# Kernel tuning notes

Hardware: AMD Instinct MI355X
Metric: run time of the kernel (lower is better)

## Reference

```python
import jax, jax.numpy as jnp
import numpy as np

NEG_SLOPE = 0.2    # DenseGATConv attention leaky_relu slope (PyG default)
ACT_SLOPE = 0.01   # block activation LeakyReLU slope
HEADS = 3


def setup_inputs() -> dict:
    key = jax.random.key(0)
    B, N, D0, D1, D2, H = 512, 128, 128, 64, 64, HEADS
    ks = jax.random.split(key, 7)
    x = jax.random.normal(ks[0], (B * N, D0), jnp.float32)
    # equal-sized graphs: sorted graph ids, N atoms per graph
    batch_mask = jnp.repeat(jnp.arange(B, dtype=jnp.int32), N)
    s0 = 1.0 / np.sqrt(D0)
    s1 = 1.0 / np.sqrt(D1)
    s2 = 1.0 / np.sqrt(D2)
    W1 = jax.random.normal(ks[1], (D0, H * D1), jnp.float32) * s0
    att_src1 = jax.random.normal(ks[2], (H, D1), jnp.float32) * s1
    att_dst1 = jax.random.normal(ks[3], (H, D1), jnp.float32) * s1
    b1 = jnp.zeros((D1,), jnp.float32)
    W2 = jax.random.normal(ks[4], (D1, H * D2), jnp.float32) * s1
    att_src2 = jax.random.normal(ks[5], (H, D2), jnp.float32) * s2
    att_dst2 = jax.random.normal(ks[6], (H, D2), jnp.float32) * s2
    b2 = jnp.zeros((D2,), jnp.float32)
    return dict(x=x, batch_mask=batch_mask, W1=W1, att_src1=att_src1,
                att_dst1=att_dst1, b1=b1, W2=W2, att_src2=att_src2,
                att_dst2=att_dst2, b2=b2, batch_size=B, n_max=N)


def _dense_gat(x, adj, W, a_src, a_dst, b):
    # x: [B, N, Din], adj: [B, N, N] (self-loops already set). concat=False.
    B, N, _ = x.shape
    H, C = a_src.shape
    h = (x @ W).reshape(B, N, H, C)                       # lin (no bias)
    a_s = jnp.einsum('bnhc,hc->bnh', h, a_src)            # per-node src score
    a_d = jnp.einsum('bnhc,hc->bnh', h, a_dst)            # per-node dst score
    alpha = a_s[:, None, :, :] + a_d[:, :, None, :]       # [B, i, j, H]
    alpha = jax.nn.leaky_relu(alpha, NEG_SLOPE)
    alpha = jnp.where(adj[..., None] == 0, -jnp.inf, alpha)
    alpha = jax.nn.softmax(alpha, axis=2)                 # over source j
    out = jnp.einsum('bijh,bjhc->bihc', alpha, h)         # [B, N, H, C]
    return out.mean(axis=2) + b                           # concat=False -> head mean


def reference(x, batch_mask, W1, att_src1, att_dst1, b1,
              W2, att_src2, att_dst2, b2, batch_size, n_max):
    total, D0 = x.shape
    counts = jnp.bincount(batch_mask, length=batch_size)          # atoms per graph
    starts = jnp.cumsum(counts) - counts
    pos = jnp.arange(total) - starts[batch_mask]                  # slot within graph
    # to_dense_batch
    xd = jnp.zeros((batch_size, n_max, D0), x.dtype).at[batch_mask, pos].set(x)
    node_in = jnp.arange(n_max)[None, :] < counts[:, None]        # [B, N] valid mask
    # block adjacency: fully connected within each graph, diag zeroed...
    adj = (node_in[:, :, None] & node_in[:, None, :]).astype(x.dtype)
    # ...then DenseGATConv add_loop=True re-sets the full diagonal to 1
    adj = jnp.where(jnp.eye(n_max, dtype=bool), jnp.asarray(1.0, x.dtype), adj)
    h = _dense_gat(xd, adj, W1, att_src1, att_dst1, b1)
    h = jax.nn.leaky_relu(h, ACT_SLOPE)
    h = _dense_gat(h, adj, W2, att_src2, att_dst2, b2)
    h = jax.nn.leaky_relu(h, ACT_SLOPE)
    return jnp.sum(h, axis=1)                                     # sum pooling -> [B, D2]
```

## Files before the change

kernel.cpp:

```cpp
#include <hip/hip_runtime.h>
#include <stdint.h>

#define NROW 128
#define HCC  192

typedef __attribute__((ext_vector_type(8))) __bf16 bf16x8;
typedef __attribute__((ext_vector_type(4))) float  f32x4;

static __device__ __forceinline__ uint16_t f2bf(float f) {
    union { float f; uint32_t i; } v; v.f = f;
    uint32_t x = v.i;
    return (uint16_t)((x + 0x7FFFu + ((x >> 16) & 1u)) >> 16);
}
static __device__ __forceinline__ uint16_t bfbits(float f) {
    __bf16 h = (__bf16)f;
    union { __bf16 h; uint16_t u; } c; c.h = h; return c.u;
}

__global__ __launch_bounds__(256)
void prep_kernel(const float* __restrict__ W1, const float* __restrict__ W2,
                 uint16_t* __restrict__ wT1, uint16_t* __restrict__ wT2)
{
    int bid = blockIdx.x, t = threadIdx.x;
    if (bid < 96) {
        int idx = bid * 256 + t;
        int c = idx >> 7, k = idx & 127;
        wT1[c * 128 + k] = f2bf(W1[k * HCC + c]);
    } else {
        int idx = (bid - 96) * 256 + t;
        int c = idx >> 6, k = idx & 63;
        wT2[c * 64 + k] = f2bf(W2[k * HCC + c]);
    }
}

#define HS 136
#define S2 72

static __device__ __forceinline__
void scores_and_hT(const f32x4* hacc, const float* attS, const float* attD,
                   uint16_t* hT, float* as_s, float* ad_s,
                   int i0, int lr, int lg)
{
    float ps[12], pd[12];
#pragma unroll
    for (int q = 0; q < 12; ++q) { ps[q] = 0.f; pd[q] = 0.f; }
#pragma unroll
    for (int f = 0; f < 12; ++f) {
        int hd = f >> 2;
        float av = attS[f * 16 + lr], dv = attD[f * 16 + lr];
#pragma unroll
        for (int r = 0; r < 4; ++r) {
            float hv = hacc[f][r];
            ps[hd * 4 + r] += hv * av;
            pd[hd * 4 + r] += hv * dv;
        }
    }
#pragma unroll
    for (int off = 1; off < 16; off <<= 1)
#pragma unroll
        for (int q = 0; q < 12; ++q) {
            ps[q] += __shfl_xor(ps[q], off);
            pd[q] += __shfl_xor(pd[q], off);
        }
    if (lr == 0) {
#pragma unroll
        for (int hd = 0; hd < 3; ++hd)
#pragma unroll
            for (int r = 0; r < 4; ++r) {
                as_s[hd * 128 + i0 + lg * 4 + r] = ps[hd * 4 + r];
                ad_s[hd * 128 + i0 + lg * 4 + r] = pd[hd * 4 + r];
            }
    }
#pragma unroll
    for (int f = 0; f < 12; ++f) {
        uint32_t p0 = (uint32_t)bfbits(hacc[f][0]) | ((uint32_t)bfbits(hacc[f][1]) << 16);
        uint32_t p1 = (uint32_t)bfbits(hacc[f][2]) | ((uint32_t)bfbits(hacc[f][3]) << 16);
        *(uint2*)&hT[(f * 16 + lr) * HS + i0 + lg * 4] = make_uint2(p0, p1);
    }
}

static __device__ __forceinline__
void softmax_pv(const uint16_t* hT, const float* as_s, const float* ad_s,
                f32x4* oacc, int i0, int l, int lr, int lg)
{
#pragma unroll
    for (int f = 0; f < 4; ++f) oacc[f] = (f32x4){0.f, 0.f, 0.f, 0.f};

    float mxh[3];
#pragma unroll
    for (int hd = 0; hd < 3; ++hd) {
        float a0 = as_s[hd * 128 + l], a1 = as_s[hd * 128 + l + 64];
        mxh[hd] = fmaxf(a0, a1);
    }
#pragma unroll
    for (int off = 1; off < 64; off <<= 1)
#pragma unroll
        for (int hd = 0; hd < 3; ++hd) mxh[hd] = fmaxf(mxh[hd], __shfl_xor(mxh[hd], off));

    for (int hd = 0; hd < 3; ++hd) {
        float ad = ad_s[hd * 128 + i0 + lr];
        float m0 = mxh[hd] + ad;
        float mi = fmaxf(m0, 0.2f * m0);

        float e[4][8];
        float zp = 0.f;
#pragma unroll
        for (int q = 0; q < 4; ++q) {
            float4 s0 = *(const float4*)&as_s[hd * 128 + q * 32 + lg * 8];
            float4 s1 = *(const float4*)&as_s[hd * 128 + q * 32 + lg * 8 + 4];
            float sv[8] = {s0.x, s0.y, s0.z, s0.w, s1.x, s1.y, s1.z, s1.w};
#pragma unroll
            for (int m = 0; m < 8; ++m) {
                float tt = sv[m] + ad;
                tt = fmaxf(tt, 0.2f * tt);
                float ev = __expf(tt - mi);
                e[q][m] = ev; zp += ev;
            }
        }
        zp += __shfl_xor(zp, 16);
        zp += __shfl_xor(zp, 32);
        float inv = 1.0f / zp;
        bf16x8 ap[4];
#pragma unroll
        for (int q = 0; q < 4; ++q)
#pragma unroll
            for (int m = 0; m < 8; ++m) ap[q][m] = (__bf16)(e[q][m] * inv);
#pragma unroll
        for (int q = 0; q < 4; ++q)
#pragma unroll
            for (int f = 0; f < 4; ++f) {
                bf16x8 bfv = *(const bf16x8*)&hT[(hd * 64 + f * 16 + lr) * HS + q * 32 + lg * 8];
                oacc[f] = __builtin_amdgcn_mfma_f32_16x16x32_bf16(ap[q], bfv, oacc[f], 0, 0, 0);
            }
    }
}

__global__ __launch_bounds__(512, 4)
void fused_kernel(const float* __restrict__ x,
                  const uint16_t* __restrict__ wT1g, const uint16_t* __restrict__ wT2g,
                  const float* __restrict__ as1g, const float* __restrict__ ad1g,
                  const float* __restrict__ b1g,
                  const float* __restrict__ as2g, const float* __restrict__ ad2g,
                  const float* __restrict__ b2g,
                  float* __restrict__ outp)
{
    __shared__ __align__(16) uint16_t buf[HCC * HS];
    __shared__ __align__(16) float as_s[3 * 128];
    __shared__ __align__(16) float ad_s[3 * 128];
    __shared__ float attS[2][HCC], attD[2][HCC], bia[2][64];
    __shared__ float pool_s[8 * 64];

    uint16_t* wT1l = buf;
    uint16_t* hT   = buf;
    uint16_t* x2T  = buf;
    uint16_t* wT2l = buf + 128 * S2;

    const int b = blockIdx.x, t = threadIdx.x;
    const int w = t >> 6, l = t & 63, lr = l & 15, lg = l >> 4;
    const int i0 = w * 16;

    bf16x8 afr[4];
    {
        const float* xg = x + ((long)b * NROW + i0 + lr) * 128;
        float4 r0[4], r1[4];
#pragma unroll
        for (int q = 0; q < 4; ++q) {
            r0[q] = *(const float4*)(xg + q * 32 + lg * 8);
            r1[q] = *(const float4*)(xg + q * 32 + lg * 8 + 4);
        }
#pragma unroll
        for (int q = 0; q < 4; ++q) {
            bf16x8 a;
            a[0] = (__bf16)r0[q].x; a[1] = (__bf16)r0[q].y;
            a[2] = (__bf16)r0[q].z; a[3] = (__bf16)r0[q].w;
            a[4] = (__bf16)r1[q].x; a[5] = (__bf16)r1[q].y;
            a[6] = (__bf16)r1[q].z; a[7] = (__bf16)r1[q].w;
            afr[q] = a;
        }
    }
#pragma unroll
    for (int p = 0; p < 6; ++p) {
        int idx = t + p * 512; int row = idx >> 4; int c8 = (idx & 15) * 8;
        *(uint4*)&wT1l[row * HS + c8] = *(const uint4*)(wT1g + row * 128 + c8);
    }
    if (t < 192)      { attS[0][t] = as1g[t]; attD[0][t] = ad1g[t]; }
    else if (t < 384) { attS[1][t - 192] = as2g[t - 192]; attD[1][t - 192] = ad2g[t - 192]; }
    else if (t < 448) bia[0][t - 384] = b1g[t - 384];
    else              bia[1][t - 448] = b2g[t - 448];
    __syncthreads();

    f32x4 hacc[12];
#pragma unroll
    for (int f = 0; f < 12; ++f) hacc[f] = (f32x4){0.f, 0.f, 0.f, 0.f};
#pragma unroll
    for (int q = 0; q < 4; ++q) {
#pragma unroll
        for (int f = 0; f < 12; ++f) {
            bf16x8 bfv = *(const bf16x8*)&wT1l[(f * 16 + lr) * HS + q * 32 + lg * 8];
            hacc[f] = __builtin_amdgcn_mfma_f32_16x16x32_bf16(afr[q], bfv, hacc[f], 0, 0, 0);
        }
    }
    __syncthreads();

    scores_and_hT(hacc, attS[0], attD[0], hT, as_s, ad_s, i0, lr, lg);
    __syncthreads();

    uint4 wpre[3];
#pragma unroll
    for (int p = 0; p < 3; ++p) {
        int idx = t + p * 512; int row = idx >> 3; int c8 = (idx & 7) * 8;
        wpre[p] = *(const uint4*)(wT2g + row * 64 + c8);
    }

    f32x4 oacc[4];
    softmax_pv(hT, as_s, ad_s, oacc, i0, l, lr, lg);
    __syncthreads();

    {
        const float inv3 = 1.f / 3.f;
#pragma unroll
        for (int f = 0; f < 4; ++f) {
            int c = f * 16 + lr;
            float bv = bia[0][c];
#pragma unroll
            for (int r = 0; r < 4; ++r) {
                float v = oacc[f][r] * inv3 + bv;
                v = fmaxf(v, 0.01f * v);
                x2T[(i0 + lg * 4 + r) * S2 + c] = bfbits(v);
            }
        }
#pragma unroll
        for (int p = 0; p < 3; ++p) {
            int idx = t + p * 512; int row = idx >> 3; int c8 = (idx & 7) * 8;
            *(uint4*)&wT2l[row * S2 + c8] = wpre[p];
        }
    }
    __syncthreads();

#pragma unroll
    for (int f = 0; f < 12; ++f) hacc[f] = (f32x4){0.f, 0.f, 0.f, 0.f};
#pragma unroll
    for (int q = 0; q < 2; ++q) {
        bf16x8 af = *(const bf16x8*)&x2T[(i0 + lr) * S2 + q * 32 + lg * 8];
#pragma unroll
        for (int f = 0; f < 12; ++f) {
            bf16x8 bfv = *(const bf16x8*)&wT2l[(f * 16 + lr) * S2 + q * 32 + lg * 8];
            hacc[f] = __builtin_amdgcn_mfma_f32_16x16x32_bf16(af, bfv, hacc[f], 0, 0, 0);
        }
    }
    __syncthreads();

    scores_and_hT(hacc, attS[1], attD[1], hT, as_s, ad_s, i0, lr, lg);
    __syncthreads();

    softmax_pv(hT, as_s, ad_s, oacc, i0, l, lr, lg);

    {
        const float inv3 = 1.f / 3.f;
#pragma unroll
        for (int f = 0; f < 4; ++f) {
            int c = f * 16 + lr;
            float bv = bia[1][c];
            float s = 0.f;
#pragma unroll
            for (int r = 0; r < 4; ++r) {
                float v = oacc[f][r] * inv3 + bv;
                v = fmaxf(v, 0.01f * v);
                s += v;
            }
            s += __shfl_xor(s, 16);
            s += __shfl_xor(s, 32);
            if (lg == 0) pool_s[w * 64 + c] = s;
        }
    }
    __syncthreads();
    if (t < 64) {
        float s = 0.f;
#pragma unroll
        for (int q = 0; q < 8; ++q) s += pool_s[q * 64 + t];
        outp[(long)b * 64 + t] = s;
    }
}

extern "C" void kernel_launch(void* const* d_in, const int* in_sizes, int n_in,
                              void* d_out, int out_size, void* d_ws, size_t ws_size,
                              hipStream_t stream)
{
    const float* x   = (const float*)d_in[0];
    const float* W1  = (const float*)d_in[2];
    const float* as1 = (const float*)d_in[3];
    const float* ad1 = (const float*)d_in[4];
    const float* b1  = (const float*)d_in[5];
    const float* W2  = (const float*)d_in[6];
    const float* as2 = (const float*)d_in[7];
    const float* ad2 = (const float*)d_in[8];
    const float* b2  = (const float*)d_in[9];

    uint16_t* wT1 = (uint16_t*)d_ws;
    uint16_t* wT2 = wT1 + 192 * 128;

    prep_kernel<<<144, 256, 0, stream>>>(W1, W2, wT1, wT2);
    fused_kernel<<<512, 512, 0, stream>>>(x, wT1, wT2, as1, ad1, b1, as2, ad2, b2,
                                          (float*)d_out);
}
```

Baseline: 131.7 us.

## Fold attention vectors into weights and defer softmax normalization

Precomputes W·att_src and W·att_dst per head in the prep kernel (scaled by log2e) and appends them as 16 extra output columns, so the attention scores come out of the projection MFMA instead of a shuffle-reduction pass. Softmax now uses exp2 and applies the 1/(3·Z) normalization after the PV MFMA through a per-row reciprocal shuffle, which also absorbs the head-mean scaling. This removes the score reductions and the per-element normalization multiplies, at the cost of one extra MFMA column tile per projection. Scores are now rounded to bf16, which reduces their precision.

```diff
diff --git a/kernel.cpp b/kernel.cpp
--- a/kernel.cpp
+++ b/kernel.cpp
@@ -2,7 +2,6 @@
 #include <stdint.h>
 
 #define NROW 128
-#define HCC  192
 
 typedef __attribute__((ext_vector_type(8))) __bf16 bf16x8;
 typedef __attribute__((ext_vector_type(4))) float  f32x4;
@@ -16,20 +15,74 @@
     __bf16 h = (__bf16)f;
     union { __bf16 h; uint16_t u; } c; c.h = h; return c.u;
 }
+static __device__ __forceinline__ float fexp2(float x) {
+#if __has_builtin(__builtin_amdgcn_exp2f)
+    return __builtin_amdgcn_exp2f(x);
+#else
+    return exp2f(x);
+#endif
+}
+static __device__ __forceinline__ float frcp(float x) {
+#if __has_builtin(__builtin_amdgcn_rcpf)
+    return __builtin_amdgcn_rcpf(x);
+#else
+    return 1.0f / x;
+#endif
+}
 
 __global__ __launch_bounds__(256)
-void prep_kernel(const float* __restrict__ W1, const float* __restrict__ W2,
-                 uint16_t* __restrict__ wT1, uint16_t* __restrict__ wT2)
-{
+void prep_kernel(const float* __restrict__ W1, const float* __restrict__ as1,
+                 const float* __restrict__ ad1,
+                 const float* __restrict__ W2, const float* __restrict__ as2,
+                 const float* __restrict__ ad2,
+                 uint16_t* __restrict__ wT1x, uint16_t* __restrict__ wT2x)
+{
+    constexpr float LOG2E = 1.4426950408889634f;
     int bid = blockIdx.x, t = threadIdx.x;
     if (bid < 96) {
         int idx = bid * 256 + t;
         int c = idx >> 7, k = idx & 127;
-        wT1[c * 128 + k] = f2bf(W1[k * HCC + c]);
-    } else {
+        wT1x[c * 128 + k] = f2bf(W1[k * 192 + c]);
+    } else if (bid < 144) {
         int idx = (bid - 96) * 256 + t;
         int c = idx >> 6, k = idx & 63;
-        wT2[c * 64 + k] = f2bf(W2[k * HCC + c]);
+        wT2x[c * 64 + k] = f2bf(W2[k * 192 + c]);
+    } else if (bid == 144) {
+#pragma unroll
+        for (int e = 0; e < 3; ++e) {
+            int idx = t + e * 256;
+            if (idx < 768) {
+                int j = idx >> 7, k = idx & 127, hd = j >> 1;
+                const float* av = (j & 1) ? ad1 : as1;
+                float s = 0.f;
+                for (int c = 0; c < 64; ++c)
+                    s += W1[k * 192 + hd * 64 + c] * av[hd * 64 + c];
+                wT1x[(192 + j) * 128 + k] = f2bf(s * LOG2E);
+            }
+        }
+#pragma unroll
+        for (int e = 0; e < 5; ++e) {
+            int idx = t + e * 256;
+            if (idx < 1280) wT1x[198 * 128 + idx] = 0;
+        }
+    } else {
+#pragma unroll
+        for (int e = 0; e < 2; ++e) {
+            int idx = t + e * 256;
+            if (idx < 384) {
+                int j = idx >> 6, k = idx & 63, hd = j >> 1;
+                const float* av = (j & 1) ? ad2 : as2;
+                float s = 0.f;
+                for (int c = 0; c < 64; ++c)
+                    s += W2[k * 192 + hd * 64 + c] * av[hd * 64 + c];
+                wT2x[(192 + j) * 64 + k] = f2bf(s * LOG2E);
+            }
+        }
+#pragma unroll
+        for (int e = 0; e < 3; ++e) {
+            int idx = t + e * 256;
+            if (idx < 640) wT2x[198 * 64 + idx] = 0;
+        }
     }
 }
 
@@ -37,39 +90,15 @@
 #define S2 72
 
 static __device__ __forceinline__
-void scores_and_hT(const f32x4* hacc, const float* attS, const float* attD,
-                   uint16_t* hT, float* as_s, float* ad_s,
+void scores_and_hT(const f32x4* hacc, uint16_t* hT, float* as_s, float* ad_s,
                    int i0, int lr, int lg)
 {
-    float ps[12], pd[12];
-#pragma unroll
-    for (int q = 0; q < 12; ++q) { ps[q] = 0.f; pd[q] = 0.f; }
-#pragma unroll
-    for (int f = 0; f < 12; ++f) {
-        int hd = f >> 2;
-        float av = attS[f * 16 + lr], dv = attD[f * 16 + lr];
-#pragma unroll
-        for (int r = 0; r < 4; ++r) {
-            float hv = hacc[f][r];
-            ps[hd * 4 + r] += hv * av;
-            pd[hd * 4 + r] += hv * dv;
-        }
-    }
-#pragma unroll
-    for (int off = 1; off < 16; off <<= 1)
-#pragma unroll
-        for (int q = 0; q < 12; ++q) {
-            ps[q] += __shfl_xor(ps[q], off);
-            pd[q] += __shfl_xor(pd[q], off);
-        }
-    if (lr == 0) {
-#pragma unroll
-        for (int hd = 0; hd < 3; ++hd)
-#pragma unroll
-            for (int r = 0; r < 4; ++r) {
-                as_s[hd * 128 + i0 + lg * 4 + r] = ps[hd * 4 + r];
-                ad_s[hd * 128 + i0 + lg * 4 + r] = pd[hd * 4 + r];
-            }
+    if (lr < 6) {
+        float* dst = (lr & 1) ? ad_s : as_s;
+        int hd = lr >> 1;
+#pragma unroll
+        for (int r = 0; r < 4; ++r)
+            dst[hd * 128 + i0 + lg * 4 + r] = hacc[12][r];
     }
 #pragma unroll
     for (int f = 0; f < 12; ++f) {
@@ -88,10 +117,8 @@
 
     float mxh[3];
 #pragma unroll
-    for (int hd = 0; hd < 3; ++hd) {
-        float a0 = as_s[hd * 128 + l], a1 = as_s[hd * 128 + l + 64];
-        mxh[hd] = fmaxf(a0, a1);
-    }
+    for (int hd = 0; hd < 3; ++hd)
+        mxh[hd] = fmaxf(as_s[hd * 128 + l], as_s[hd * 128 + l + 64]);
 #pragma unroll
     for (int off = 1; off < 64; off <<= 1)
 #pragma unroll
@@ -101,8 +128,7 @@
         float ad = ad_s[hd * 128 + i0 + lr];
         float m0 = mxh[hd] + ad;
         float mi = fmaxf(m0, 0.2f * m0);
-
-        float e[4][8];
+        bf16x8 ap[4];
         float zp = 0.f;
 #pragma unroll
         for (int q = 0; q < 4; ++q) {
@@ -113,41 +139,45 @@
             for (int m = 0; m < 8; ++m) {
                 float tt = sv[m] + ad;
                 tt = fmaxf(tt, 0.2f * tt);
-                float ev = __expf(tt - mi);
-                e[q][m] = ev; zp += ev;
+                float ev = fexp2(tt - mi);
+                zp += ev;
+                ap[q][m] = (__bf16)ev;
             }
         }
         zp += __shfl_xor(zp, 16);
         zp += __shfl_xor(zp, 32);
-        float inv = 1.0f / zp;
-        bf16x8 ap[4];
-#pragma unroll
-        for (int q = 0; q < 4; ++q)
-#pragma unroll
-            for (int m = 0; m < 8; ++m) ap[q][m] = (__bf16)(e[q][m] * inv);
+        float inv = frcp(3.0f * zp);
+
+        f32x4 tacc[4];
+#pragma unroll
+        for (int f = 0; f < 4; ++f) tacc[f] = (f32x4){0.f, 0.f, 0.f, 0.f};
 #pragma unroll
         for (int q = 0; q < 4; ++q)
 #pragma unroll
             for (int f = 0; f < 4; ++f) {
                 bf16x8 bfv = *(const bf16x8*)&hT[(hd * 64 + f * 16 + lr) * HS + q * 32 + lg * 8];
-                oacc[f] = __builtin_amdgcn_mfma_f32_16x16x32_bf16(ap[q], bfv, oacc[f], 0, 0, 0);
-            }
+                tacc[f] = __builtin_amdgcn_mfma_f32_16x16x32_bf16(ap[q], bfv, tacc[f], 0, 0, 0);
+            }
+        float invr[4];
+#pragma unroll
+        for (int r = 0; r < 4; ++r) invr[r] = __shfl(inv, lg * 4 + r);
+#pragma unroll
+        for (int f = 0; f < 4; ++f)
+#pragma unroll
+            for (int r = 0; r < 4; ++r) oacc[f][r] += tacc[f][r] * invr[r];
     }
 }
 
 __global__ __launch_bounds__(512, 4)
 void fused_kernel(const float* __restrict__ x,
                   const uint16_t* __restrict__ wT1g, const uint16_t* __restrict__ wT2g,
-                  const float* __restrict__ as1g, const float* __restrict__ ad1g,
-                  const float* __restrict__ b1g,
-                  const float* __restrict__ as2g, const float* __restrict__ ad2g,
-                  const float* __restrict__ b2g,
+                  const float* __restrict__ b1g, const float* __restrict__ b2g,
                   float* __restrict__ outp)
 {
-    __shared__ __align__(16) uint16_t buf[HCC * HS];
+    __shared__ __align__(16) uint16_t buf[208 * HS];
     __shared__ __align__(16) float as_s[3 * 128];
     __shared__ __align__(16) float ad_s[3 * 128];
-    __shared__ float attS[2][HCC], attD[2][HCC], bia[2][64];
+    __shared__ float bia[2][64];
     __shared__ float pool_s[8 * 64];
 
     uint16_t* wT1l = buf;
@@ -179,52 +209,56 @@
         }
     }
 #pragma unroll
-    for (int p = 0; p < 6; ++p) {
-        int idx = t + p * 512; int row = idx >> 4; int c8 = (idx & 15) * 8;
-        *(uint4*)&wT1l[row * HS + c8] = *(const uint4*)(wT1g + row * 128 + c8);
-    }
-    if (t < 192)      { attS[0][t] = as1g[t]; attD[0][t] = ad1g[t]; }
-    else if (t < 384) { attS[1][t - 192] = as2g[t - 192]; attD[1][t - 192] = ad2g[t - 192]; }
-    else if (t < 448) bia[0][t - 384] = b1g[t - 384];
-    else              bia[1][t - 448] = b2g[t - 448];
-    __syncthreads();
-
-    f32x4 hacc[12];
-#pragma unroll
-    for (int f = 0; f < 12; ++f) hacc[f] = (f32x4){0.f, 0.f, 0.f, 0.f};
+    for (int p = 0; p < 7; ++p) {
+        int idx = t + p * 512;
+        if (idx < 3328) {
+            int row = idx >> 4, c8 = (idx & 15) * 8;
+            *(uint4*)&wT1l[row * HS + c8] = *(const uint4*)(wT1g + row * 128 + c8);
+        }
+    }
+    if (t < 64) bia[0][t] = b1g[t];
+    else if (t < 128) bia[1][t - 64] = b2g[t - 64];
+    __syncthreads();
+
+    f32x4 hacc[13];
+#pragma unroll
+    for (int f = 0; f < 13; ++f) hacc[f] = (f32x4){0.f, 0.f, 0.f, 0.f};
 #pragma unroll
     for (int q = 0; q < 4; ++q) {
 #pragma unroll
-        for (int f = 0; f < 12; ++f) {
+        for (int f = 0; f < 13; ++f) {
             bf16x8 bfv = *(const bf16x8*)&wT1l[(f * 16 + lr) * HS + q * 32 + lg * 8];
             hacc[f] = __builtin_amdgcn_mfma_f32_16x16x32_bf16(afr[q], bfv, hacc[f], 0, 0, 0);
         }
     }
     __syncthreads();
 
-    scores_and_hT(hacc, attS[0], attD[0], hT, as_s, ad_s, i0, lr, lg);
-    __syncthreads();
-
-    uint4 wpre[3];
+    scores_and_hT(hacc, hT, as_s, ad_s, i0, lr, lg);
+    __syncthreads();
+
+    uint4 wpre[4];
 #pragma unroll
     for (int p = 0; p < 3; ++p) {
         int idx = t + p * 512; int row = idx >> 3; int c8 = (idx & 7) * 8;
         wpre[p] = *(const uint4*)(wT2g + row * 64 + c8);
     }
+    if (t < 128) {
+        int idx = t + 1536; int row = idx >> 3; int c8 = (idx & 7) * 8;
+        wpre[3] = *(const uint4*)(wT2g + row * 64 + c8);
+    }
 
     f32x4 oacc[4];
     softmax_pv(hT, as_s, ad_s, oacc, i0, l, lr, lg);
     __syncthreads();
 
     {
-        const float inv3 = 1.f / 3.f;
 #pragma unroll
         for (int f = 0; f < 4; ++f) {
             int c = f * 16 + lr;
             float bv = bia[0][c];
 #pragma unroll
             for (int r = 0; r < 4; ++r) {
-                float v = oacc[f][r] * inv3 + bv;
+                float v = oacc[f][r] + bv;
                 v = fmaxf(v, 0.01f * v);
                 x2T[(i0 + lg * 4 + r) * S2 + c] = bfbits(v);
             }
@@ -234,44 +268,45 @@
             int idx = t + p * 512; int row = idx >> 3; int c8 = (idx & 7) * 8;
             *(uint4*)&wT2l[row * S2 + c8] = wpre[p];
         }
-    }
-    __syncthreads();
-
-#pragma unroll
-    for (int f = 0; f < 12; ++f) hacc[f] = (f32x4){0.f, 0.f, 0.f, 0.f};
+        if (t < 128) {
+            int idx = t + 1536; int row = idx >> 3; int c8 = (idx & 7) * 8;
+            *(uint4*)&wT2l[row * S2 + c8] = wpre[3];
+        }
+    }
+    __syncthreads();
+
+#pragma unroll
+    for (int f = 0; f < 13; ++f) hacc[f] = (f32x4){0.f, 0.f, 0.f, 0.f};
 #pragma unroll
     for (int q = 0; q < 2; ++q) {
         bf16x8 af = *(const bf16x8*)&x2T[(i0 + lr) * S2 + q * 32 + lg * 8];
 #pragma unroll
-        for (int f = 0; f < 12; ++f) {
+        for (int f = 0; f < 13; ++f) {
             bf16x8 bfv = *(const bf16x8*)&wT2l[(f * 16 + lr) * S2 + q * 32 + lg * 8];
             hacc[f] = __builtin_amdgcn_mfma_f32_16x16x32_bf16(af, bfv, hacc[f], 0, 0, 0);
         }
     }
     __syncthreads();
 
-    scores_and_hT(hacc, attS[1], attD[1], hT, as_s, ad_s, i0, lr, lg);
+    scores_and_hT(hacc, hT, as_s, ad_s, i0, lr, lg);
     __syncthreads();
 
     softmax_pv(hT, as_s, ad_s, oacc, i0, l, lr, lg);
 
-    {
-        const float inv3 = 1.f / 3.f;
-#pragma unroll
-        for (int f = 0; f < 4; ++f) {
-            int c = f * 16 + lr;
-            float bv = bia[1][c];
-            float s = 0.f;
-#pragma unroll
-            for (int r = 0; r < 4; ++r) {
-                float v = oacc[f][r] * inv3 + bv;
-                v = fmaxf(v, 0.01f * v);
-                s += v;
-            }
-            s += __shfl_xor(s, 16);
-            s += __shfl_xor(s, 32);
-            if (lg == 0) pool_s[w * 64 + c] = s;
-        }
+#pragma unroll
+    for (int f = 0; f < 4; ++f) {
+        int c = f * 16 + lr;
+        float bv = bia[1][c];
+        float s = 0.f;
+#pragma unroll
+        for (int r = 0; r < 4; ++r) {
+            float v = oacc[f][r] + bv;
+            v = fmaxf(v, 0.01f * v);
+            s += v;
+        }
+        s += __shfl_xor(s, 16);
+        s += __shfl_xor(s, 32);
+        if (lg == 0) pool_s[w * 64 + c] = s;
     }
     __syncthreads();
     if (t < 64) {
@@ -296,10 +331,9 @@
     const float* ad2 = (const float*)d_in[8];
     const float* b2  = (const float*)d_in[9];
 
-    uint16_t* wT1 = (uint16_t*)d_ws;
-    uint16_t* wT2 = wT1 + 192 * 128;
-
-    prep_kernel<<<144, 256, 0, stream>>>(W1, W2, wT1, wT2);
-    fused_kernel<<<512, 512, 0, stream>>>(x, wT1, wT2, as1, ad1, b1, as2, ad2, b2,
-                                          (float*)d_out);
-}
+    uint16_t* wT1x = (uint16_t*)d_ws;
+    uint16_t* wT2x = wT1x + 208 * 128;
+
+    prep_kernel<<<146, 256, 0, stream>>>(W1, as1, ad1, W2, as2, ad2, wT1x, wT2x);
+    fused_kernel<<<512, 512, 0, stream>>>(x, wT1x, wT2x, b1, b2, (float*)d_out);
+}
```

Measured after the change: 127.7 us. 3.0% less time.
